# Kernel tuning notes

Hardware: AMD Instinct MI355X
Metric: run time of the kernel (lower is better)

## Reference

```python
import jax, jax.numpy as jnp
import numpy as np

B, S, D, H = 4, 4096, 1024, 64


def setup_inputs() -> dict:
    key = jax.random.key(0)
    k1, k2, k3, k4 = jax.random.split(key, 4)
    x = jax.random.normal(k1, (B, S, D), dtype=jnp.float32)
    # nn.Linear(D, H, bias=False) weights, stored as [D, H] for x @ W
    scale = 1.0 / np.sqrt(D)
    Wk = jax.random.uniform(k2, (D, H), dtype=jnp.float32, minval=-scale, maxval=scale)
    Wq = jax.random.uniform(k3, (D, H), dtype=jnp.float32, minval=-scale, maxval=scale)
    Wv = jax.random.uniform(k4, (D, H), dtype=jnp.float32, minval=-scale, maxval=scale)
    return {"x": x, "Wq": Wq, "Wk": Wk, "Wv": Wv}


def reference(x, Wq, Wk, Wv):
    # x: [B, S, D]
    head_size = Wq.shape[-1]
    q = jnp.einsum('bsd,dh->bsh', x, Wq)
    k = jnp.einsum('bsd,dh->bsh', x, Wk)
    v = jnp.einsum('bsd,dh->bsh', x, Wv)
    scores = jnp.einsum('bqh,bkh->bqk', q, k) * (head_size ** -0.5)  # [B,S,S]
    S_ = x.shape[1]
    causal = jnp.tril(jnp.ones((S_, S_), dtype=bool))
    scores = jnp.where(causal[None, :, :], scores, -jnp.inf)
    attn = jax.nn.softmax(scores, axis=-1)
    return jnp.einsum('bqk,bkh->bqh', attn, v)  # [B,S,H]
```

## Files before the change

### kernel.cpp

```cpp
#include <hip/hip_runtime.h>

typedef __attribute__((ext_vector_type(8))) short bf16x8;
typedef __attribute__((ext_vector_type(4))) short bf16x4;
typedef __attribute__((ext_vector_type(4))) float f32x4;

#define MFMA16(A, Bv, C) __builtin_amdgcn_mfma_f32_16x16x32_bf16((A), (Bv), (C), 0, 0, 0)

static constexpr int NB = 4, NS = 4096, ND = 1024, NH = 64;

__device__ __forceinline__ unsigned short f2bf(float f) {
    union { float f; unsigned int u; } x; x.f = f;
    unsigned int r = x.u + 0x7fffu + ((x.u >> 16) & 1u);
    return (unsigned short)(r >> 16);
}

__device__ __forceinline__ void gload_lds16(const void* g, void* l) {
    __builtin_amdgcn_global_load_lds((const __attribute__((address_space(1))) void*)g,
                                     (__attribute__((address_space(3))) void*)l, 16, 0, 0);
}

__global__ __launch_bounds__(256) void wconv(
    const float* __restrict__ Wq, const float* __restrict__ Wk,
    const float* __restrict__ Wv, unsigned short* __restrict__ wT)
{
    int mn = blockIdx.x;
    int m = mn >> 6, n = mn & 63;
    const float* W = (m == 0) ? Wq : (m == 1) ? Wk : Wv;
    unsigned short* dst = wT + (size_t)mn * ND;
    for (int k = threadIdx.x; k < ND; k += 256)
        dst[k] = f2bf(W[(size_t)k * NH + n]);
}

__global__ __launch_bounds__(512) void qkv_proj(
    const float* __restrict__ x, const unsigned short* __restrict__ wT,
    unsigned short* __restrict__ qo, unsigned short* __restrict__ ko,
    unsigned short* __restrict__ vt)
{
    __shared__ unsigned short Ws[2][192][64];
    __shared__ unsigned short Xs[2][32][72];
    __shared__ unsigned short Ls[32][72];

    const int tid  = threadIdx.x;
    const int lane = tid & 63;
    const int w    = tid >> 6;
    const int lr   = lane & 15;
    const int lg   = lane >> 4;
    const int mg   = w >> 2;
    const int cg   = w & 3;
    const int mbase = blockIdx.x * 32;

    const int wr8 = lane >> 3;
    const int wck = (lane & 7) ^ wr8;
    const int xrow = tid & 31;
    const int xcg  = tid >> 5;

    f32x4 acc[3];
    #pragma unroll
    for (int f = 0; f < 3; ++f) acc[f] = (f32x4){0.f, 0.f, 0.f, 0.f};

    const float* xsrc = x + (size_t)(mbase + xrow) * ND + xcg * 4;

    #define STAGE_W(buf, kb)                                                         \
        do {                                                                         \
            _Pragma("unroll")                                                        \
            for (int i_ = 0; i_ < 3; ++i_) {                                         \
                int rb_ = w * 24 + i_ * 8;                                           \
                gload_lds16(wT + (size_t)(rb_ + wr8) * ND + (kb) + wck * 8,          \
                            &Ws[buf][rb_][0]);                                       \
            }                                                                        \
        } while (0)

    #define LOADX(kb) do { xr = *(const float4*)(xsrc + (kb)); } while (0)

    #define WRITEX(buf)                                                              \
        do {                                                                         \
            bf16x4 p_;                                                               \
            p_[0] = (short)f2bf(xr.x); p_[1] = (short)f2bf(xr.y);                    \
            p_[2] = (short)f2bf(xr.z); p_[3] = (short)f2bf(xr.w);                    \
            *(bf16x4*)&Xs[buf][xrow][xcg * 4] = p_;                                  \
        } while (0)

    float4 xr;
    STAGE_W(0, 0);
    LOADX(0);
    WRITEX(0);
    __syncthreads();

    for (int kt = 0; kt < 16; ++kt) {
        const int cur = kt & 1;
        if (kt + 1 < 16) {
            STAGE_W(cur ^ 1, (kt + 1) * 64);
            LOADX((kt + 1) * 64);
        }

        #pragma unroll
        for (int kk = 0; kk < 2; ++kk) {
            bf16x8 af = *(const bf16x8*)&Xs[cur][mg * 16 + lr][(kk * 4 + lg) * 8];
            #pragma unroll
            for (int f = 0; f < 3; ++f) {
                int row = cg * 48 + f * 16 + lr;
                bf16x8 bfr = *(const bf16x8*)&Ws[cur][row][((kk * 4 + lg) ^ (lr & 7)) * 8];
                acc[f] = MFMA16(af, bfr, acc[f]);
            }
        }

        if (kt + 1 < 16) WRITEX(cur ^ 1);
        __syncthreads();
    }

    #pragma unroll
    for (int f = 0; f < 3; ++f) {
        int b16 = cg * 3 + f;
        int sel = b16 >> 2;
        int col = (b16 & 3) * 16 + lr;
        #pragma unroll
        for (int rr = 0; rr < 4; ++rr) {
            int mrow = mg * 16 + lg * 4 + rr;
            float v = acc[f][rr];
            if (sel == 0)
                qo[(size_t)(mbase + mrow) * NH + col] = f2bf(v * 0.125f);
            else if (sel == 1)
                ko[(size_t)(mbase + mrow) * NH + col] = f2bf(v);
            else
                Ls[mrow][col] = f2bf(v);
        }
    }
    __syncthreads();
    {
        int h  = tid >> 3;
        int s4 = (tid & 7) * 4;
        bf16x4 v0;
        #pragma unroll
        for (int jj = 0; jj < 4; ++jj) v0[jj] = (short)Ls[s4 + jj][h];
        int b_ = mbase >> 12;
        int sb = (mbase & (NS - 1)) + s4;
        *(bf16x4*)(vt + ((size_t)(b_ * NH + h)) * NS + sb) = v0;
    }
    #undef STAGE_W
    #undef LOADX
    #undef WRITEX
}

__global__ __launch_bounds__(256) void attn_part(
    const unsigned short* __restrict__ q, const unsigned short* __restrict__ k,
    const unsigned short* __restrict__ vt, float* __restrict__ pO,
    float* __restrict__ pm, float* __restrict__ pl)
{
    __shared__ unsigned short Kt[2][64][64];
    __shared__ unsigned short Vt[2][64][64];
    __shared__ unsigned short Ps[4][16][72];

    const int bid = blockIdx.x;
    const int b = bid & 3;
    const int j = (bid >> 2) & 63;
    const int c = bid >> 8;
    if (c > (j >> 3)) return;
    const int ntile = (j + 1 - c * 8 < 8) ? (j + 1 - c * 8) : 8;
    const int tg0 = c * 8;

    const int tid  = threadIdx.x;
    const int lane = tid & 63;
    const int w    = tid >> 6;
    const int lr   = lane & 15;
    const int lg   = lane >> 4;
    const size_t bq = (size_t)b * NS;
    const int qb = j * 64;

    const int srow = lane >> 3;
    const int schk = (lane & 7) ^ srow;

    #define STAGEKV(buf, tg)                                                          \
        do {                                                                          \
            int kvb_ = (tg) * 64;                                                     \
            if (w < 2) {                                                              \
                _Pragma("unroll")                                                     \
                for (int i_ = 0; i_ < 4; ++i_) {                                      \
                    int rb_ = w * 32 + i_ * 8;                                        \
                    const unsigned short* src_ =                                      \
                        k + (bq + kvb_ + rb_ + srow) * NH + schk * 8;                 \
                    gload_lds16(src_, &Kt[buf][rb_][0]);                              \
                }                                                                     \
            } else {                                                                  \
                _Pragma("unroll")                                                     \
                for (int i_ = 0; i_ < 4; ++i_) {                                      \
                    int rb_ = (w - 2) * 32 + i_ * 8;                                  \
                    const unsigned short* src_ =                                      \
                        vt + ((size_t)(b * NH + rb_ + srow)) * NS + kvb_ + schk * 8;  \
                    gload_lds16(src_, &Vt[buf][rb_][0]);                              \
                }                                                                     \
            }                                                                         \
        } while (0)

    bf16x8 qf0, qf1;
    {
        const unsigned short* qp = q + (bq + qb + w * 16 + lr) * NH + lg * 8;
        qf0 = *(const bf16x8*)qp;
        qf1 = *(const bf16x8*)(qp + 32);
    }

    f32x4 O[4];
    #pragma unroll
    for (int i = 0; i < 4; ++i) O[i] = (f32x4){0.f, 0.f, 0.f, 0.f};
    float mrow = -3.0e38f, lsum = 0.f;

    STAGEKV(0, tg0);
    __syncthreads();

    int cur = 0;
    for (int t = 0; t < ntile; ++t) {
        const int tg = tg0 + t;
        STAGEKV(cur ^ 1, (t + 1 < ntile) ? tg + 1 : tg0);

        f32x4 sf[4];
        #pragma unroll
        for (int f = 0; f < 4; ++f) {
            f32x4 s = (f32x4){0.f, 0.f, 0.f, 0.f};
            int row = f * 16 + lr;
            bf16x8 kb0 = *(const bf16x8*)&Kt[cur][row][((lg    ) ^ (lr & 7)) * 8];
            bf16x8 kb1 = *(const bf16x8*)&Kt[cur][row][((lg + 4) ^ (lr & 7)) * 8];
            s = MFMA16(kb0, qf0, s);
            s = MFMA16(kb1, qf1, s);
            sf[f] = s;
        }

        if (tg == j) {
            #pragma unroll
            for (int f = 0; f < 4; ++f)
                #pragma unroll
                for (int r = 0; r < 4; ++r) {
                    int kvl = f * 16 + lg * 4 + r;
                    int ql  = w * 16 + lr;
                    if (kvl > ql) sf[f][r] = -3.0e38f;
                }
        }

        float pmx = fmaxf(fmaxf(fmaxf(sf[0][0], sf[0][1]), fmaxf(sf[0][2], sf[0][3])),
                          fmaxf(fmaxf(sf[1][0], sf[1][1]), fmaxf(sf[1][2], sf[1][3])));
        float pmx2 = fmaxf(fmaxf(fmaxf(sf[2][0], sf[2][1]), fmaxf(sf[2][2], sf[2][3])),
                           fmaxf(fmaxf(sf[3][0], sf[3][1]), fmaxf(sf[3][2], sf[3][3])));
        pmx = fmaxf(pmx, pmx2);
        pmx = fmaxf(pmx, __shfl_xor(pmx, 16));
        pmx = fmaxf(pmx, __shfl_xor(pmx, 32));
        float mnew = fmaxf(mrow, pmx);
        float corr = __expf(mrow - mnew);
        mrow = mnew;
        float rs = 0.f;
        #pragma unroll
        for (int f = 0; f < 4; ++f)
            #pragma unroll
            for (int r = 0; r < 4; ++r) {
                float p = __expf(sf[f][r] - mnew);
                sf[f][r] = p;
                rs += p;
            }
        rs += __shfl_xor(rs, 16);
        rs += __shfl_xor(rs, 32);
        lsum = lsum * corr + rs;
        #pragma unroll
        for (int hf = 0; hf < 4; ++hf) O[hf] *= corr;

        #pragma unroll
        for (int f = 0; f < 4; ++f)
            #pragma unroll
            for (int r = 0; r < 4; ++r)
                Ps[w][lr][f * 16 + lg * 4 + r] = f2bf(sf[f][r]);

        bf16x8 pb0 = *(const bf16x8*)&Ps[w][lr][lg * 8];
        bf16x8 pb1 = *(const bf16x8*)&Ps[w][lr][32 + lg * 8];

        #pragma unroll
        for (int hf = 0; hf < 4; ++hf) {
            int row = hf * 16 + lr;
            bf16x8 vb0 = *(const bf16x8*)&Vt[cur][row][((lg    ) ^ (lr & 7)) * 8];
            bf16x8 vb1 = *(const bf16x8*)&Vt[cur][row][((lg + 4) ^ (lr & 7)) * 8];
            O[hf] = MFMA16(vb0, pb0, O[hf]);
            O[hf] = MFMA16(vb1, pb1, O[hf]);
        }

        __syncthreads();
        cur ^= 1;
    }

    const int a8 = j >> 3, r8 = j & 7;
    const int pidx = b * 288 + (a8 + 1) * (4 * a8 + r8) + c;
    float* Po = pO + (size_t)pidx * 4096;
    #pragma unroll
    for (int hf = 0; hf < 4; ++hf)
        *(f32x4*)&Po[(w * 16 + lr) * 64 + hf * 16 + lg * 4] = O[hf];
    if (lane < 16) {
        pm[pidx * 64 + w * 16 + lane] = mrow;
        pl[pidx * 64 + w * 16 + lane] = lsum;
    }
    #undef STAGEKV
}

__global__ __launch_bounds__(256) void attn_merge(
    const float* __restrict__ pO, const float* __restrict__ pm,
    const float* __restrict__ pl, float* __restrict__ out)
{
    const int bid = blockIdx.x;
    const int b = bid & 3, j = bid >> 2;
    const int nch = (j >> 3) + 1;
    const int a8 = j >> 3, r8 = j & 7;
    const int pbase = b * 288 + (a8 + 1) * (4 * a8 + r8);
    const int tid = threadIdx.x;
    const int row = tid >> 2, hq = (tid & 3) * 16;

    float M = -3.0e38f, L = 0.f;
    f32x4 acc0 = {0,0,0,0}, acc1 = {0,0,0,0}, acc2 = {0,0,0,0}, acc3 = {0,0,0,0};
    for (int cc = 0; cc < nch; ++cc) {
        int pidx = pbase + cc;
        float mc = pm[pidx * 64 + row];
        float lc = pl[pidx * 64 + row];
        const f32x4* po = (const f32x4*)(pO + (size_t)pidx * 4096 + row * 64 + hq);
        float Mn = fmaxf(M, mc);
        float sO = __expf(M - Mn), sN = __expf(mc - Mn);
        L = L * sO + lc * sN;
        acc0 = acc0 * sO + po[0] * sN;
        acc1 = acc1 * sO + po[1] * sN;
        acc2 = acc2 * sO + po[2] * sN;
        acc3 = acc3 * sO + po[3] * sN;
        M = Mn;
    }
    float inv = 1.f / L;
    float* op = out + ((size_t)b * NS + (size_t)j * 64 + row) * NH + hq;
    *(f32x4*)(op + 0)  = acc0 * inv;
    *(f32x4*)(op + 4)  = acc1 * inv;
    *(f32x4*)(op + 8)  = acc2 * inv;
    *(f32x4*)(op + 12) = acc3 * inv;
}

extern "C" void kernel_launch(void* const* d_in, const int* in_sizes, int n_in,
                              void* d_out, int out_size, void* d_ws, size_t ws_size,
                              hipStream_t stream)
{
    const float* x  = (const float*)d_in[0];
    const float* Wq = (const float*)d_in[1];
    const float* Wk = (const float*)d_in[2];
    const float* Wv = (const float*)d_in[3];
    float* out = (float*)d_out;

    const size_t n = (size_t)NB * NS * NH;
    unsigned short* qb_ = (unsigned short*)d_ws;
    unsigned short* kb_ = qb_ + n;
    unsigned short* vT  = kb_ + n;
    unsigned short* wT  = vT + n;
    float* pO  = (float*)(wT + 192 * 1024);
    float* pm_ = pO + (size_t)1152 * 4096;
    float* pl_ = pm_ + 1152 * 64;

    wconv<<<dim3(192), dim3(256), 0, stream>>>(Wq, Wk, Wv, wT);
    qkv_proj<<<dim3(512), dim3(512), 0, stream>>>(x, wT, qb_, kb_, vT);
    attn_part<<<dim3(2048), dim3(256), 0, stream>>>(qb_, kb_, vT, pO, pm_, pl_);
    attn_merge<<<dim3(256), dim3(256), 0, stream>>>(pO, pm_, pl_, out);
}
```

Baseline: 64.09 us.

## Split QKV projection across two N-halves per row tile with swizzled X staging

The QKV projection kernel now launches 1024 blocks of 256 threads. Each block computes half of the 192 output columns for a 32-row tile, where before one block of 512 threads did all of them. X is loaded as 8 floats per thread and stored to LDS as bf16x8 with an XOR swizzle that replaces the padding. Only the V half performs the transposed V write. This is meant to raise occupancy and CU coverage for the projection, at the cost of every x tile being read and converted twice, once by each block.

Measured after the change: 76.84 us. 1.2x slower.

```diff
diff --git a/kernel.cpp b/kernel.cpp
--- a/kernel.cpp
+++ b/kernel.cpp
@@ -31,13 +31,13 @@
         dst[k] = f2bf(W[(size_t)k * NH + n]);
 }
 
-__global__ __launch_bounds__(512) void qkv_proj(
+__global__ __launch_bounds__(256) void qkv_proj(
     const float* __restrict__ x, const unsigned short* __restrict__ wT,
     unsigned short* __restrict__ qo, unsigned short* __restrict__ ko,
     unsigned short* __restrict__ vt)
 {
-    __shared__ unsigned short Ws[2][192][64];
-    __shared__ unsigned short Xs[2][32][72];
+    __shared__ unsigned short Ws[2][96][64];
+    __shared__ unsigned short Xs[2][32][64];
     __shared__ unsigned short Ls[32][72];
 
     const int tid  = threadIdx.x;
@@ -45,42 +45,50 @@
     const int w    = tid >> 6;
     const int lr   = lane & 15;
     const int lg   = lane >> 4;
-    const int mg   = w >> 2;
-    const int cg   = w & 3;
-    const int mbase = blockIdx.x * 32;
+    const int mg   = w >> 1;
+    const int cg   = w & 1;
+    const int mbase = (blockIdx.x >> 1) * 32;
+    const int nh    = blockIdx.x & 1;
+    const int nbase = nh * 96;
 
     const int wr8 = lane >> 3;
     const int wck = (lane & 7) ^ wr8;
     const int xrow = tid & 31;
-    const int xcg  = tid >> 5;
+    const int xg   = tid >> 5;
 
     f32x4 acc[3];
     #pragma unroll
     for (int f = 0; f < 3; ++f) acc[f] = (f32x4){0.f, 0.f, 0.f, 0.f};
 
-    const float* xsrc = x + (size_t)(mbase + xrow) * ND + xcg * 4;
+    const float* xsrc = x + (size_t)(mbase + xrow) * ND + xg * 8;
 
     #define STAGE_W(buf, kb)                                                         \
         do {                                                                         \
             _Pragma("unroll")                                                        \
             for (int i_ = 0; i_ < 3; ++i_) {                                         \
                 int rb_ = w * 24 + i_ * 8;                                           \
-                gload_lds16(wT + (size_t)(rb_ + wr8) * ND + (kb) + wck * 8,          \
+                gload_lds16(wT + (size_t)(nbase + rb_ + wr8) * ND + (kb) + wck * 8,  \
                             &Ws[buf][rb_][0]);                                       \
             }                                                                        \
         } while (0)
 
-    #define LOADX(kb) do { xr = *(const float4*)(xsrc + (kb)); } while (0)
+    #define LOADX(kb)                                                                \
+        do {                                                                         \
+            xr0 = *(const float4*)(xsrc + (kb));                                     \
+            xr1 = *(const float4*)(xsrc + (kb) + 4);                                 \
+        } while (0)
 
     #define WRITEX(buf)                                                              \
         do {                                                                         \
-            bf16x4 p_;                                                               \
-            p_[0] = (short)f2bf(xr.x); p_[1] = (short)f2bf(xr.y);                    \
-            p_[2] = (short)f2bf(xr.z); p_[3] = (short)f2bf(xr.w);                    \
-            *(bf16x4*)&Xs[buf][xrow][xcg * 4] = p_;                                  \
+            bf16x8 p_;                                                               \
+            p_[0] = (short)f2bf(xr0.x); p_[1] = (short)f2bf(xr0.y);                  \
+            p_[2] = (short)f2bf(xr0.z); p_[3] = (short)f2bf(xr0.w);                  \
+            p_[4] = (short)f2bf(xr1.x); p_[5] = (short)f2bf(xr1.y);                  \
+            p_[6] = (short)f2bf(xr1.z); p_[7] = (short)f2bf(xr1.w);                  \
+            *(bf16x8*)&Xs[buf][xrow][(xg ^ (xrow & 7)) * 8] = p_;                    \
         } while (0)
 
-    float4 xr;
+    float4 xr0, xr1;
     STAGE_W(0, 0);
     LOADX(0);
     WRITEX(0);
@@ -95,11 +103,12 @@
 
         #pragma unroll
         for (int kk = 0; kk < 2; ++kk) {
-            bf16x8 af = *(const bf16x8*)&Xs[cur][mg * 16 + lr][(kk * 4 + lg) * 8];
+            int row = mg * 16 + lr;
+            bf16x8 af = *(const bf16x8*)&Xs[cur][row][((kk * 4 + lg) ^ (lr & 7)) * 8];
             #pragma unroll
             for (int f = 0; f < 3; ++f) {
-                int row = cg * 48 + f * 16 + lr;
-                bf16x8 bfr = *(const bf16x8*)&Ws[cur][row][((kk * 4 + lg) ^ (lr & 7)) * 8];
+                int nrow = cg * 48 + f * 16 + lr;
+                bf16x8 bfr = *(const bf16x8*)&Ws[cur][nrow][((kk * 4 + lg) ^ (lr & 7)) * 8];
                 acc[f] = MFMA16(af, bfr, acc[f]);
             }
         }
@@ -110,7 +119,7 @@
 
     #pragma unroll
     for (int f = 0; f < 3; ++f) {
-        int b16 = cg * 3 + f;
+        int b16 = nh * 6 + cg * 3 + f;
         int sel = b16 >> 2;
         int col = (b16 & 3) * 16 + lr;
         #pragma unroll
@@ -126,15 +135,15 @@
         }
     }
     __syncthreads();
-    {
-        int h  = tid >> 3;
-        int s4 = (tid & 7) * 4;
-        bf16x4 v0;
-        #pragma unroll
-        for (int jj = 0; jj < 4; ++jj) v0[jj] = (short)Ls[s4 + jj][h];
+    if (nh == 1) {
+        int h  = tid >> 2;
+        int s8 = (tid & 3) * 8;
+        bf16x8 v0;
+        #pragma unroll
+        for (int jj = 0; jj < 8; ++jj) v0[jj] = (short)Ls[s8 + jj][h];
         int b_ = mbase >> 12;
-        int sb = (mbase & (NS - 1)) + s4;
-        *(bf16x4*)(vt + ((size_t)(b_ * NH + h)) * NS + sb) = v0;
+        int sb = (mbase & (NS - 1)) + s8;
+        *(bf16x8*)(vt + ((size_t)(b_ * NH + h)) * NS + sb) = v0;
     }
     #undef STAGE_W
     #undef LOADX
@@ -350,7 +359,7 @@
     float* pl_ = pm_ + 1152 * 64;
 
     wconv<<<dim3(192), dim3(256), 0, stream>>>(Wq, Wk, Wv, wT);
-    qkv_proj<<<dim3(512), dim3(512), 0, stream>>>(x, wT, qb_, kb_, vT);
+    qkv_proj<<<dim3(1024), dim3(256), 0, stream>>>(x, wT, qb_, kb_, vT);
     attn_part<<<dim3(2048), dim3(256), 0, stream>>>(qb_, kb_, vT, pO, pm_, pl_);
     attn_merge<<<dim3(256), dim3(256), 0, stream>>>(pO, pm_, pl_, out);
 }
```

## Deepen x prefetch to three register buffers with explicit vmcnt-based barriers

Applied to the files above, without the earlier changes.

The QKV projection kernel now keeps three float4 register buffers of x in flight, prefetching three k-tiles ahead instead of one. The loop is fully unrolled, and each __syncthreads is replaced with a manual s_waitcnt vmcnt(N) plus s_barrier, fenced by sched_barrier, so the waits no longer drain every outstanding global load. The aim is to hide global load latency in the projection GEMM. In exchange it uses more registers and relies on hand-counted vmcnt values, which could be fragile if the compiler reorders or emits extra memory operations.

Measured after the change: 65.37 us, median of 2. 2.0% more time.

```diff
diff --git a/kernel.cpp b/kernel.cpp
--- a/kernel.cpp
+++ b/kernel.cpp
@@ -70,27 +70,47 @@
             }                                                                        \
         } while (0)
 
-    #define LOADX(kb) do { xr = *(const float4*)(xsrc + (kb)); } while (0)
-
-    #define WRITEX(buf)                                                              \
+    #define LOADX(dst, kt_) do { dst = *(const float4*)(xsrc + (kt_) * 64); } while (0)
+
+    #define WRITEX(buf, g)                                                           \
         do {                                                                         \
             bf16x4 p_;                                                               \
-            p_[0] = (short)f2bf(xr.x); p_[1] = (short)f2bf(xr.y);                    \
-            p_[2] = (short)f2bf(xr.z); p_[3] = (short)f2bf(xr.w);                    \
+            p_[0] = (short)f2bf((g).x); p_[1] = (short)f2bf((g).y);                  \
+            p_[2] = (short)f2bf((g).z); p_[3] = (short)f2bf((g).w);                  \
             *(bf16x4*)&Xs[buf][xrow][xcg * 4] = p_;                                  \
         } while (0)
 
-    float4 xr;
+    #define FENCE() __builtin_amdgcn_sched_barrier(0)
+    #define REGION_SYNC(M)                                                           \
+        do {                                                                         \
+            FENCE();                                                                 \
+            asm volatile("s_waitcnt vmcnt(" #M ")" ::: "memory");                    \
+            FENCE();                                                                 \
+            __builtin_amdgcn_s_barrier();                                            \
+            FENCE();                                                                 \
+        } while (0)
+
+    float4 xg0, xg1, xg2;
     STAGE_W(0, 0);
-    LOADX(0);
-    WRITEX(0);
-    __syncthreads();
-
+    FENCE();
+    LOADX(xg0, 0); LOADX(xg1, 1); LOADX(xg2, 2);
+    WRITEX(0, xg0);
+    asm volatile("s_waitcnt lgkmcnt(0)" ::: "memory");
+    FENCE();
+
+    #pragma unroll
     for (int kt = 0; kt < 16; ++kt) {
+        if (kt == 0)       REGION_SYNC(2);
+        else if (kt <= 13) REGION_SYNC(1);
+        else               REGION_SYNC(0);
+
         const int cur = kt & 1;
-        if (kt + 1 < 16) {
-            STAGE_W(cur ^ 1, (kt + 1) * 64);
-            LOADX((kt + 1) * 64);
+        if (kt + 1 < 16) STAGE_W(cur ^ 1, (kt + 1) * 64);
+        FENCE();
+        if (kt + 3 < 16) {
+            if ((kt + 3) % 3 == 0)      LOADX(xg0, kt + 3);
+            else if ((kt + 3) % 3 == 1) LOADX(xg1, kt + 3);
+            else                        LOADX(xg2, kt + 3);
         }
 
         #pragma unroll
@@ -104,8 +124,13 @@
             }
         }
 
-        if (kt + 1 < 16) WRITEX(cur ^ 1);
-        __syncthreads();
+        if (kt + 1 < 16) {
+            if ((kt + 1) % 3 == 0)      WRITEX(cur ^ 1, xg0);
+            else if ((kt + 1) % 3 == 1) WRITEX(cur ^ 1, xg1);
+            else                        WRITEX(cur ^ 1, xg2);
+        }
+        asm volatile("s_waitcnt lgkmcnt(0)" ::: "memory");
+        FENCE();
     }
 
     #pragma unroll
@@ -139,6 +164,8 @@
     #undef STAGE_W
     #undef LOADX
     #undef WRITEX
+    #undef FENCE
+    #undef REGION_SYNC
 }
 
 __global__ __launch_bounds__(256) void attn_part(
```

## Fuse split-KV merge into attention kernel via last-block atomic counter

Applied to the files above, without the earlier changes.

Removes the separate attn_merge launch. Each query tile's partial blocks bump an atomic counter, and the last block to finish does the log-sum-exp merge and writes the output. Tiles with a single chunk normalize and write the output directly, skipping the partial buffers. This cuts one kernel launch plus the partial-buffer round trip for the first 8 query tiles, at the cost of thread fences, an atomic, and an added memset call.

Measured after the change: 220.8 us. +244.6%, slower.

```diff
diff --git a/kernel.cpp b/kernel.cpp
--- a/kernel.cpp
+++ b/kernel.cpp
@@ -144,17 +144,20 @@
 __global__ __launch_bounds__(256) void attn_part(
     const unsigned short* __restrict__ q, const unsigned short* __restrict__ k,
     const unsigned short* __restrict__ vt, float* __restrict__ pO,
-    float* __restrict__ pm, float* __restrict__ pl)
+    float* __restrict__ pm, float* __restrict__ pl,
+    int* __restrict__ cnt, float* __restrict__ out)
 {
     __shared__ unsigned short Kt[2][64][64];
     __shared__ unsigned short Vt[2][64][64];
     __shared__ unsigned short Ps[4][16][72];
+    __shared__ int lastflag;
 
     const int bid = blockIdx.x;
     const int b = bid & 3;
     const int j = (bid >> 2) & 63;
     const int c = bid >> 8;
     if (c > (j >> 3)) return;
+    const int nch = (j >> 3) + 1;
     const int ntile = (j + 1 - c * 8 < 8) ? (j + 1 - c * 8) : 8;
     const int tg0 = c * 8;
 
@@ -281,8 +284,20 @@
         cur ^= 1;
     }
 
+    if (nch == 1) {
+        float inv = 1.f / lsum;
+        float* op = out + (bq + qb + w * 16 + lr) * NH;
+        #pragma unroll
+        for (int hf = 0; hf < 4; ++hf) {
+            f32x4 o = O[hf] * inv;
+            *(f32x4*)&op[hf * 16 + lg * 4] = o;
+        }
+        return;
+    }
+
     const int a8 = j >> 3, r8 = j & 7;
-    const int pidx = b * 288 + (a8 + 1) * (4 * a8 + r8) + c;
+    const int pbase = b * 288 + (a8 + 1) * (4 * a8 + r8);
+    const int pidx = pbase + c;
     float* Po = pO + (size_t)pidx * 4096;
     #pragma unroll
     for (int hf = 0; hf < 4; ++hf)
@@ -291,43 +306,43 @@
         pm[pidx * 64 + w * 16 + lane] = mrow;
         pl[pidx * 64 + w * 16 + lane] = lsum;
     }
+
+    __threadfence();
+    __syncthreads();
+    if (tid == 0) {
+        int prev = atomicAdd(&cnt[b * 64 + j], 1);
+        lastflag = (prev == nch - 1);
+    }
+    __syncthreads();
+    if (!lastflag) return;
+
+    __threadfence();
+    {
+        const int row = tid >> 2, hq = (tid & 3) * 16;
+        float M = -3.0e38f, Lm = 0.f;
+        f32x4 a0 = {0,0,0,0}, a1 = {0,0,0,0}, a2 = {0,0,0,0}, a3 = {0,0,0,0};
+        for (int cc = 0; cc < nch; ++cc) {
+            int pp = pbase + cc;
+            float mc = pm[pp * 64 + row];
+            float lc = pl[pp * 64 + row];
+            const f32x4* po = (const f32x4*)(pO + (size_t)pp * 4096 + row * 64 + hq);
+            float Mn = fmaxf(M, mc);
+            float sO = __expf(M - Mn), sN = __expf(mc - Mn);
+            Lm = Lm * sO + lc * sN;
+            a0 = a0 * sO + po[0] * sN;
+            a1 = a1 * sO + po[1] * sN;
+            a2 = a2 * sO + po[2] * sN;
+            a3 = a3 * sO + po[3] * sN;
+            M = Mn;
+        }
+        float inv = 1.f / Lm;
+        float* op = out + (bq + qb + row) * NH + hq;
+        *(f32x4*)(op + 0)  = a0 * inv;
+        *(f32x4*)(op + 4)  = a1 * inv;
+        *(f32x4*)(op + 8)  = a2 * inv;
+        *(f32x4*)(op + 12) = a3 * inv;
+    }
     #undef STAGEKV
-}
-
-__global__ __launch_bounds__(256) void attn_merge(
-    const float* __restrict__ pO, const float* __restrict__ pm,
-    const float* __restrict__ pl, float* __restrict__ out)
-{
-    const int bid = blockIdx.x;
-    const int b = bid & 3, j = bid >> 2;
-    const int nch = (j >> 3) + 1;
-    const int a8 = j >> 3, r8 = j & 7;
-    const int pbase = b * 288 + (a8 + 1) * (4 * a8 + r8);
-    const int tid = threadIdx.x;
-    const int row = tid >> 2, hq = (tid & 3) * 16;
-
-    float M = -3.0e38f, L = 0.f;
-    f32x4 acc0 = {0,0,0,0}, acc1 = {0,0,0,0}, acc2 = {0,0,0,0}, acc3 = {0,0,0,0};
-    for (int cc = 0; cc < nch; ++cc) {
-        int pidx = pbase + cc;
-        float mc = pm[pidx * 64 + row];
-        float lc = pl[pidx * 64 + row];
-        const f32x4* po = (const f32x4*)(pO + (size_t)pidx * 4096 + row * 64 + hq);
-        float Mn = fmaxf(M, mc);
-        float sO = __expf(M - Mn), sN = __expf(mc - Mn);
-        L = L * sO + lc * sN;
-        acc0 = acc0 * sO + po[0] * sN;
-        acc1 = acc1 * sO + po[1] * sN;
-        acc2 = acc2 * sO + po[2] * sN;
-        acc3 = acc3 * sO + po[3] * sN;
-        M = Mn;
-    }
-    float inv = 1.f / L;
-    float* op = out + ((size_t)b * NS + (size_t)j * 64 + row) * NH + hq;
-    *(f32x4*)(op + 0)  = acc0 * inv;
-    *(f32x4*)(op + 4)  = acc1 * inv;
-    *(f32x4*)(op + 8)  = acc2 * inv;
-    *(f32x4*)(op + 12) = acc3 * inv;
 }
 
 extern "C" void kernel_launch(void* const* d_in, const int* in_sizes, int n_in,
@@ -348,9 +363,10 @@
     float* pO  = (float*)(wT + 192 * 1024);
     float* pm_ = pO + (size_t)1152 * 4096;
     float* pl_ = pm_ + 1152 * 64;
-
+    int*   cnt = (int*)(pl_ + 1152 * 64);
+
+    hipMemsetAsync(cnt, 0, 256 * sizeof(int), stream);
     wconv<<<dim3(192), dim3(256), 0, stream>>>(Wq, Wk, Wv, wT);
     qkv_proj<<<dim3(512), dim3(512), 0, stream>>>(x, wT, qb_, kb_, vT);
-    attn_part<<<dim3(2048), dim3(256), 0, stream>>>(qb_, kb_, vT, pO, pm_, pl_);
-    attn_merge<<<dim3(256), dim3(256), 0, stream>>>(pO, pm_, pl_, out);
-}
+    attn_part<<<dim3(2048), dim3(256), 0, stream>>>(qb_, kb_, vT, pO, pm_, pl_, cnt, out);
+}
```
